# Performance work log

Hardware: AMD Instinct MI355X
Metric: run time of the kernel (lower is better)

## Reference

```python
import jax, jax.numpy as jnp
import numpy as np

B, T, TWO_H = 64, 512, 1024  # batch, prev decoding steps, 2*hidden_dim


def setup_inputs() -> dict:
    key = jax.random.key(0)
    k1, k2, k3 = jax.random.split(key, 3)
    h_d_t = jax.random.normal(k1, (B, TWO_H), dtype=jnp.float32)
    prev_h_dec = jax.random.normal(k2, (B, T, TWO_H), dtype=jnp.float32)
    # nn.Bilinear(2H, 2H, attn_dim=1) weight, trunc_norm_init_std ~ 1e-4 typical
    W = jax.random.normal(k3, (1, TWO_H, TWO_H), dtype=jnp.float32) * 1e-4
    return {"h_d_t": h_d_t, "prev_h_dec": prev_h_dec, "W": W}


def reference(h_d_t, prev_h_dec, W):
    # Bilinear score: s[b,t] = h_d_t[b] @ W[0] @ prev_h_dec[b,t]
    q = jnp.einsum('bd,de->be', h_d_t, W[0])          # (B, 2H) -- one small GEMM
    attn_score = jnp.einsum('be,bte->bt', q, prev_h_dec)  # (B, T)
    alpha_t = jax.nn.softmax(attn_score, axis=1)      # (B, T)
    ct_d = jnp.einsum('bt,btd->bd', alpha_t, prev_h_dec)  # (B, 2H)
    new_prev = jnp.concatenate([prev_h_dec, h_d_t[:, None, :]], axis=1)  # (B, T+1, 2H)
    return (ct_d, new_prev)
```

## Files before the change

### kernel.cpp

```cpp
#include <hip/hip_runtime.h>
#include <math.h>

#define BB    64
#define TT    512
#define TWOH  1024
#define TC    16
#define NCHUNK (TT / TC)
#define KSPLIT 4
#define NP_STRIDE ((TT + 1) * TWOH)

typedef float vfloat4 __attribute__((ext_vector_type(4)));


__global__ __launch_bounds__(256) void k_qgemm(const float* __restrict__ h,
                                               const float* __restrict__ W,
                                               float* __restrict__ qpart) {
    const int tid = threadIdx.x;
    const int e   = blockIdx.x * 256 + tid;
    const int b   = blockIdx.y;
    const int k   = blockIdx.z;
    const int d0  = k * (TWOH / KSPLIT);

    __shared__ float sh[TWOH / KSPLIT];
    sh[tid] = h[b * TWOH + d0 + tid];
    __syncthreads();

    const float* __restrict__ Wp = W + (size_t)d0 * TWOH + e;
    float acc = 0.f;
    #pragma unroll 16
    for (int d = 0; d < TWOH / KSPLIT; ++d)
        acc = fmaf(sh[d], Wp[(size_t)d * TWOH], acc);

    qpart[((size_t)k * BB + b) * TWOH + e] = acc;
}

__global__ __launch_bounds__(256, 4) void k_scores_ct(const float* __restrict__ prev,
                                                      const float* __restrict__ qpart,
                                                      float* __restrict__ out_np,
                                                      float* __restrict__ ws_m,
                                                      float* __restrict__ ws_l,
                                                      float* __restrict__ ws_ct) {
    const int c   = blockIdx.x;
    const int b   = blockIdx.y;
    const int t0  = c * TC;
    const int tid = threadIdx.x;
    const int lane = tid & 63;
    const int wid  = tid >> 6;

    __shared__ float s_part[TC][4];
    __shared__ float s_score[TC];

    const vfloat4* __restrict__ prow =
        (const vfloat4*)(prev + (size_t)b * TT * TWOH + (size_t)t0 * TWOH) + tid;
    vfloat4* __restrict__ nprow =
        (vfloat4*)(out_np + (size_t)b * NP_STRIDE + (size_t)t0 * TWOH) + tid;

    const vfloat4* __restrict__ qp = (const vfloat4*)qpart;
    vfloat4 q4 = qp[((size_t)0 * BB + b) * 256 + tid]
               + qp[((size_t)1 * BB + b) * 256 + tid]
               + qp[((size_t)2 * BB + b) * 256 + tid]
               + qp[((size_t)3 * BB + b) * 256 + tid];

    vfloat4 pv[TC];
    #pragma unroll
    for (int t = 0; t < TC; ++t)
        pv[t] = prow[t * 256];

    #pragma unroll
    for (int t = 0; t < TC; ++t) {
        float pd = pv[t].x * q4.x + pv[t].y * q4.y + pv[t].z * q4.z + pv[t].w * q4.w;
        #pragma unroll
        for (int off = 32; off > 0; off >>= 1)
            pd += __shfl_xor(pd, off, 64);
        if (lane == 0) s_part[t][wid] = pd;
    }
    __syncthreads();
    if (tid < TC)
        s_score[tid] = s_part[tid][0] + s_part[tid][1] + s_part[tid][2] + s_part[tid][3];
    __syncthreads();

    float m = -INFINITY;
    #pragma unroll
    for (int t = 0; t < TC; ++t) m = fmaxf(m, s_score[t]);
    float l = 0.f;
    vfloat4 ct = (vfloat4)(0.f);
    #pragma unroll
    for (int t = 0; t < TC; ++t) {
        const float w = __expf(s_score[t] - m);
        l += w;
        ct.x = fmaf(w, pv[t].x, ct.x);
        ct.y = fmaf(w, pv[t].y, ct.y);
        ct.z = fmaf(w, pv[t].z, ct.z);
        ct.w = fmaf(w, pv[t].w, ct.w);
    }
    ((vfloat4*)(ws_ct + ((size_t)b * NCHUNK + c) * TWOH))[tid] = ct;
    if (tid == 0) {
        ws_m[b * NCHUNK + c] = m;
        ws_l[b * NCHUNK + c] = l;
    }

    #pragma unroll
    for (int t = 0; t < TC; ++t)
        nprow[t * 256] = pv[t];
}

__global__ __launch_bounds__(256) void k_finalize(const float* __restrict__ h,
                                                  const float* __restrict__ ws_m,
                                                  const float* __restrict__ ws_l,
                                                  const float* __restrict__ ws_ct,
                                                  float* __restrict__ out_ct,
                                                  float* __restrict__ out_np) {
    const int tid = threadIdx.x;
    const int e   = blockIdx.x * 256 + tid;
    const int b   = blockIdx.y;

    float M = -INFINITY;
    #pragma unroll
    for (int i = 0; i < NCHUNK; ++i) M = fmaxf(M, ws_m[b * NCHUNK + i]);

    float coef[NCHUNK];
    float L = 0.f;
    #pragma unroll
    for (int i = 0; i < NCHUNK; ++i) {
        const float ce = __expf(ws_m[b * NCHUNK + i] - M);
        coef[i] = ce;
        L = fmaf(ce, ws_l[b * NCHUNK + i], L);
    }
    const float inv = 1.0f / L;

    const float* __restrict__ cp = ws_ct + (size_t)b * NCHUNK * TWOH + e;
    float acc = 0.f;
    #pragma unroll
    for (int i = 0; i < NCHUNK; ++i)
        acc = fmaf(coef[i], cp[(size_t)i * TWOH], acc);
    out_ct[b * TWOH + e] = acc * inv;

    out_np[(size_t)b * NP_STRIDE + (size_t)TT * TWOH + e] = h[b * TWOH + e];
}

extern "C" void kernel_launch(void* const* d_in, const int* in_sizes, int n_in,
                              void* d_out, int out_size, void* d_ws, size_t ws_size,
                              hipStream_t stream) {
    const float* h    = (const float*)d_in[0];
    const float* prev = (const float*)d_in[1];
    const float* W    = (const float*)d_in[2];
    float* out    = (float*)d_out;
    float* out_ct = out;
    float* out_np = out + BB * TWOH;

    float* qpart = (float*)d_ws;
    float* wsm   = qpart + KSPLIT * BB * TWOH;
    float* wsl   = wsm + BB * NCHUNK;
    float* wsc   = wsl + BB * NCHUNK;

    k_qgemm<<<dim3(4, BB, KSPLIT), 256, 0, stream>>>(h, W, qpart);
    k_scores_ct<<<dim3(NCHUNK, BB), 256, 0, stream>>>(prev, qpart, out_np, wsm, wsl, wsc);
    k_finalize<<<dim3(4, BB), 256, 0, stream>>>(h, wsm, wsl, wsc, out_ct, out_np);
}
```

Baseline: 266.6 us.

## Split fused score/context kernel into separate copy, score, and context passes

Replaces the single fused kernel, which read prev once and did scores, partial softmax, context and copy together, with five kernels. There is now a standalone bulk copy of prev into the output, a scores pass, and a context pass that uses the full softmax instead of online rescaling. A final kernel sums the per-group context partials. The q GEMM no longer splits K. This reads prev three times instead of once, roughly 384MB of extra traffic, in exchange for simpler, higher-occupancy kernels.

```diff
diff --git a/kernel.cpp b/kernel.cpp
--- a/kernel.cpp
+++ b/kernel.cpp
@@ -4,138 +4,167 @@
 #define BB    64
 #define TT    512
 #define TWOH  1024
-#define TC    16
-#define NCHUNK (TT / TC)
-#define KSPLIT 4
 #define NP_STRIDE ((TT + 1) * TWOH)
+#define TPB   64
+#define NG    (TT / TPB)
 
 typedef float vfloat4 __attribute__((ext_vector_type(4)));
 
 
 __global__ __launch_bounds__(256) void k_qgemm(const float* __restrict__ h,
                                                const float* __restrict__ W,
-                                               float* __restrict__ qpart) {
-    const int tid = threadIdx.x;
-    const int e   = blockIdx.x * 256 + tid;
-    const int b   = blockIdx.y;
-    const int k   = blockIdx.z;
-    const int d0  = k * (TWOH / KSPLIT);
-
-    __shared__ float sh[TWOH / KSPLIT];
-    sh[tid] = h[b * TWOH + d0 + tid];
-    __syncthreads();
-
-    const float* __restrict__ Wp = W + (size_t)d0 * TWOH + e;
-    float acc = 0.f;
-    #pragma unroll 16
-    for (int d = 0; d < TWOH / KSPLIT; ++d)
-        acc = fmaf(sh[d], Wp[(size_t)d * TWOH], acc);
-
-    qpart[((size_t)k * BB + b) * TWOH + e] = acc;
-}
-
-__global__ __launch_bounds__(256, 4) void k_scores_ct(const float* __restrict__ prev,
-                                                      const float* __restrict__ qpart,
-                                                      float* __restrict__ out_np,
-                                                      float* __restrict__ ws_m,
-                                                      float* __restrict__ ws_l,
-                                                      float* __restrict__ ws_ct) {
-    const int c   = blockIdx.x;
-    const int b   = blockIdx.y;
-    const int t0  = c * TC;
-    const int tid = threadIdx.x;
-    const int lane = tid & 63;
-    const int wid  = tid >> 6;
-
-    __shared__ float s_part[TC][4];
-    __shared__ float s_score[TC];
-
-    const vfloat4* __restrict__ prow =
-        (const vfloat4*)(prev + (size_t)b * TT * TWOH + (size_t)t0 * TWOH) + tid;
-    vfloat4* __restrict__ nprow =
-        (vfloat4*)(out_np + (size_t)b * NP_STRIDE + (size_t)t0 * TWOH) + tid;
-
-    const vfloat4* __restrict__ qp = (const vfloat4*)qpart;
-    vfloat4 q4 = qp[((size_t)0 * BB + b) * 256 + tid]
-               + qp[((size_t)1 * BB + b) * 256 + tid]
-               + qp[((size_t)2 * BB + b) * 256 + tid]
-               + qp[((size_t)3 * BB + b) * 256 + tid];
-
-    vfloat4 pv[TC];
-    #pragma unroll
-    for (int t = 0; t < TC; ++t)
-        pv[t] = prow[t * 256];
-
-    #pragma unroll
-    for (int t = 0; t < TC; ++t) {
-        float pd = pv[t].x * q4.x + pv[t].y * q4.y + pv[t].z * q4.z + pv[t].w * q4.w;
-        #pragma unroll
-        for (int off = 32; off > 0; off >>= 1)
-            pd += __shfl_xor(pd, off, 64);
-        if (lane == 0) s_part[t][wid] = pd;
-    }
-    __syncthreads();
-    if (tid < TC)
-        s_score[tid] = s_part[tid][0] + s_part[tid][1] + s_part[tid][2] + s_part[tid][3];
-    __syncthreads();
-
-    float m = -INFINITY;
-    #pragma unroll
-    for (int t = 0; t < TC; ++t) m = fmaxf(m, s_score[t]);
-    float l = 0.f;
-    vfloat4 ct = (vfloat4)(0.f);
-    #pragma unroll
-    for (int t = 0; t < TC; ++t) {
-        const float w = __expf(s_score[t] - m);
-        l += w;
-        ct.x = fmaf(w, pv[t].x, ct.x);
-        ct.y = fmaf(w, pv[t].y, ct.y);
-        ct.z = fmaf(w, pv[t].z, ct.z);
-        ct.w = fmaf(w, pv[t].w, ct.w);
-    }
-    ((vfloat4*)(ws_ct + ((size_t)b * NCHUNK + c) * TWOH))[tid] = ct;
-    if (tid == 0) {
-        ws_m[b * NCHUNK + c] = m;
-        ws_l[b * NCHUNK + c] = l;
-    }
-
-    #pragma unroll
-    for (int t = 0; t < TC; ++t)
-        nprow[t * 256] = pv[t];
-}
-
-__global__ __launch_bounds__(256) void k_finalize(const float* __restrict__ h,
-                                                  const float* __restrict__ ws_m,
-                                                  const float* __restrict__ ws_l,
-                                                  const float* __restrict__ ws_ct,
-                                                  float* __restrict__ out_ct,
-                                                  float* __restrict__ out_np) {
+                                               float* __restrict__ q) {
     const int tid = threadIdx.x;
     const int e   = blockIdx.x * 256 + tid;
     const int b   = blockIdx.y;
 
-    float M = -INFINITY;
+    __shared__ float sh[TWOH];
+    ((vfloat4*)sh)[tid] = ((const vfloat4*)(h + (size_t)b * TWOH))[tid];
+    __syncthreads();
+
+    const float* __restrict__ Wp = W + e;
+    float acc = 0.f;
+    #pragma unroll 16
+    for (int d = 0; d < TWOH; ++d)
+        acc = fmaf(sh[d], Wp[(size_t)d * TWOH], acc);
+
+    q[(size_t)b * TWOH + e] = acc;
+}
+
+__global__ __launch_bounds__(256) void k_copy(const float* __restrict__ prev,
+                                              const float* __restrict__ h,
+                                              float* __restrict__ out_np) {
+    const int gx  = blockIdx.x;
+    const int tid = threadIdx.x;
+    const vfloat4* __restrict__ in4 = (const vfloat4*)prev;
+    vfloat4* __restrict__ out4      = (vfloat4*)out_np;
+
+    if (gx < 8192) {
+        const int base = gx * 1024 + tid;
+        vfloat4 v0 = in4[base];
+        vfloat4 v1 = in4[base + 256];
+        vfloat4 v2 = in4[base + 512];
+        vfloat4 v3 = in4[base + 768];
+        const int i0 = base,       b0 = i0 >> 17;
+        const int i1 = base + 256, b1 = i1 >> 17;
+        const int i2 = base + 512, b2 = i2 >> 17;
+        const int i3 = base + 768, b3 = i3 >> 17;
+        out4[i0 + (b0 << 8)] = v0;
+        out4[i1 + (b1 << 8)] = v1;
+        out4[i2 + (b2 << 8)] = v2;
+        out4[i3 + (b3 << 8)] = v3;
+    } else {
+        const int flat = (gx - 8192) * 256 + tid;
+        const int b    = flat >> 8;
+        const int e4   = flat & 255;
+        out4[(size_t)b * (513 * 256) + 512 * 256 + e4] =
+            ((const vfloat4*)h)[flat];
+    }
+}
+
+__global__ __launch_bounds__(256, 8) void k_scores(const float* __restrict__ prev,
+                                                   const float* __restrict__ q,
+                                                   float* __restrict__ s) {
+    const int tid  = threadIdx.x;
+    const int lane = tid & 63;
+    const int wid  = tid >> 6;
+    const int b    = blockIdx.y;
+    const int t    = blockIdx.x * 4 + wid;
+
+    const vfloat4* __restrict__ pr =
+        (const vfloat4*)(prev + ((size_t)b * TT + t) * TWOH) + lane;
+    const vfloat4* __restrict__ qv =
+        (const vfloat4*)(q + (size_t)b * TWOH) + lane;
+
+    const vfloat4 v0 = pr[0],   v1 = pr[64],  v2 = pr[128], v3 = pr[192];
+    const vfloat4 q0 = qv[0],   q1 = qv[64],  q2 = qv[128], q3 = qv[192];
+
+    float d0 = v0.x * q0.x; d0 = fmaf(v0.y, q0.y, d0);
+    d0 = fmaf(v0.z, q0.z, d0); d0 = fmaf(v0.w, q0.w, d0);
+    float d1 = v1.x * q1.x; d1 = fmaf(v1.y, q1.y, d1);
+    d1 = fmaf(v1.z, q1.z, d1); d1 = fmaf(v1.w, q1.w, d1);
+    float d2 = v2.x * q2.x; d2 = fmaf(v2.y, q2.y, d2);
+    d2 = fmaf(v2.z, q2.z, d2); d2 = fmaf(v2.w, q2.w, d2);
+    float d3 = v3.x * q3.x; d3 = fmaf(v3.y, q3.y, d3);
+    d3 = fmaf(v3.z, q3.z, d3); d3 = fmaf(v3.w, q3.w, d3);
+    float pd = (d0 + d1) + (d2 + d3);
     #pragma unroll
-    for (int i = 0; i < NCHUNK; ++i) M = fmaxf(M, ws_m[b * NCHUNK + i]);
+    for (int off = 32; off > 0; off >>= 1)
+        pd += __shfl_xor(pd, off, 64);
 
-    float coef[NCHUNK];
-    float L = 0.f;
+    if (lane == 0) s[b * TT + t] = pd;
+}
+
+__global__ __launch_bounds__(256) void k_ct(const float* __restrict__ prev,
+                                            const float* __restrict__ s,
+                                            float* __restrict__ ctp) {
+    const int tid  = threadIdx.x;
+    const int lane = tid & 63;
+    const int wid  = tid >> 6;
+    const int g    = blockIdx.x;
+    const int b    = blockIdx.y;
+
+    __shared__ float ss[TT];
+    __shared__ float als[TT];
+    __shared__ float red[8];
+
+    if (tid < 128)
+        ((vfloat4*)ss)[tid] = ((const vfloat4*)(s + b * TT))[tid];
+    __syncthreads();
+
+    const float v0 = ss[tid];
+    const float v1 = ss[tid + 256];
+
+    float m2 = fmaxf(v0, v1);
     #pragma unroll
-    for (int i = 0; i < NCHUNK; ++i) {
-        const float ce = __expf(ws_m[b * NCHUNK + i] - M);
-        coef[i] = ce;
-        L = fmaf(ce, ws_l[b * NCHUNK + i], L);
-    }
+    for (int off = 32; off > 0; off >>= 1)
+        m2 = fmaxf(m2, __shfl_xor(m2, off, 64));
+    if (lane == 0) red[wid] = m2;
+    __syncthreads();
+    const float M = fmaxf(fmaxf(red[0], red[1]), fmaxf(red[2], red[3]));
+
+    const float e0 = __expf(v0 - M);
+    const float e1 = __expf(v1 - M);
+    float l2 = e0 + e1;
+    #pragma unroll
+    for (int off = 32; off > 0; off >>= 1)
+        l2 += __shfl_xor(l2, off, 64);
+    if (lane == 0) red[4 + wid] = l2;
+    __syncthreads();
+    const float L   = (red[4] + red[5]) + (red[6] + red[7]);
     const float inv = 1.0f / L;
 
-    const float* __restrict__ cp = ws_ct + (size_t)b * NCHUNK * TWOH + e;
-    float acc = 0.f;
+    als[tid]       = e0 * inv;
+    als[tid + 256] = e1 * inv;
+    __syncthreads();
+
+    const vfloat4* __restrict__ pr =
+        (const vfloat4*)(prev + ((size_t)b * TT + g * TPB) * TWOH) + tid;
+    vfloat4 acc = (vfloat4)(0.f);
+    #pragma unroll 8
+    for (int tt = 0; tt < TPB; ++tt) {
+        const float a   = als[g * TPB + tt];
+        const vfloat4 v = pr[tt * 256];
+        acc.x = fmaf(a, v.x, acc.x);
+        acc.y = fmaf(a, v.y, acc.y);
+        acc.z = fmaf(a, v.z, acc.z);
+        acc.w = fmaf(a, v.w, acc.w);
+    }
+    ((vfloat4*)ctp)[((size_t)b * NG + g) * 256 + tid] = acc;
+}
+
+__global__ __launch_bounds__(256) void k_ctcomb(const float* __restrict__ ctp,
+                                                float* __restrict__ out_ct) {
+    const int tid = threadIdx.x;
+    const int b   = blockIdx.x;
+    const vfloat4* __restrict__ cp = (const vfloat4*)ctp + (size_t)b * NG * 256 + tid;
+    vfloat4 acc = (vfloat4)(0.f);
     #pragma unroll
-    for (int i = 0; i < NCHUNK; ++i)
-        acc = fmaf(coef[i], cp[(size_t)i * TWOH], acc);
-    out_ct[b * TWOH + e] = acc * inv;
-
-    out_np[(size_t)b * NP_STRIDE + (size_t)TT * TWOH + e] = h[b * TWOH + e];
+    for (int gg = 0; gg < NG; ++gg) {
+        const vfloat4 v = cp[gg * 256];
+        acc.x += v.x; acc.y += v.y; acc.z += v.z; acc.w += v.w;
+    }
+    ((vfloat4*)out_ct)[b * 256 + tid] = acc;
 }
 
 extern "C" void kernel_launch(void* const* d_in, const int* in_sizes, int n_in,
@@ -148,12 +177,13 @@
     float* out_ct = out;
     float* out_np = out + BB * TWOH;
 
-    float* qpart = (float*)d_ws;
-    float* wsm   = qpart + KSPLIT * BB * TWOH;
-    float* wsl   = wsm + BB * NCHUNK;
-    float* wsc   = wsl + BB * NCHUNK;
+    float* q   = (float*)d_ws;
+    float* sc  = q + BB * TWOH;
+    float* ctp = sc + BB * TT;
 
-    k_qgemm<<<dim3(4, BB, KSPLIT), 256, 0, stream>>>(h, W, qpart);
-    k_scores_ct<<<dim3(NCHUNK, BB), 256, 0, stream>>>(prev, qpart, out_np, wsm, wsl, wsc);
-    k_finalize<<<dim3(4, BB), 256, 0, stream>>>(h, wsm, wsl, wsc, out_ct, out_np);
+    k_qgemm <<<dim3(4, BB),   256, 0, stream>>>(h, W, q);
+    k_copy  <<<dim3(8192 + 64), 256, 0, stream>>>(prev, h, out_np);
+    k_scores<<<dim3(128, BB), 256, 0, stream>>>(prev, q, sc);
+    k_ct    <<<dim3(NG, BB),  256, 0, stream>>>(prev, sc, ctp);
+    k_ctcomb<<<dim3(BB),      256, 0, stream>>>(ctp, out_ct);
 }
```

New measurement: 321.6 us. 20.6% more time.
